# Optimization experiments

Hardware: AMD Instinct MI355X
Metric: run time of the kernel (lower is better)

## Reference

```python
import jax, jax.numpy as jnp
import numpy as np

N_CELLS_RNA, N_GENES = 8000, 8000
N_CELLS_ATAC, N_REGIONS = 8000, 20000
N_FACTORS = 100

def setup_inputs() -> dict:
    key = jax.random.key(0)
    ks = jax.random.split(key, 10)
    return {
        "G": jax.random.uniform(ks[0], (N_CELLS_RNA, N_GENES), jnp.float32),
        "R": jax.random.uniform(ks[1], (N_CELLS_ATAC, N_REGIONS), jnp.float32),
        "A": jax.random.uniform(ks[2], (N_GENES, N_REGIONS), jnp.float32),
        "C_1": jax.random.uniform(ks[3], (N_CELLS_RNA, N_FACTORS), jnp.float32),
        "C_2": jax.random.uniform(ks[4], (N_CELLS_ATAC, N_FACTORS), jnp.float32),
        "C_g": jax.random.uniform(ks[5], (N_GENES, N_FACTORS), jnp.float32),
        "C_r": jax.random.uniform(ks[6], (N_REGIONS, N_FACTORS), jnp.float32),
        "A_g": jax.random.normal(ks[7], (N_FACTORS, N_FACTORS), jnp.float32),
        "A_r": jax.random.normal(ks[8], (N_FACTORS, N_FACTORS), jnp.float32),
        "b_g": jnp.zeros((1, N_GENES), jnp.float32),
        "b_r": jnp.zeros((1, N_REGIONS), jnp.float32),
        "b_1": jnp.zeros((N_CELLS_RNA, 1), jnp.float32),
        "b_2": jnp.zeros((N_CELLS_ATAC, 1), jnp.float32),
        "alpha": jnp.array([1000.0, 1000.0, 100.0, 10.0, 0.0], jnp.float32),
    }

def reference(G, R, A, C_1, C_2, C_g, C_r, A_g, A_r, b_g, b_r, b_1, b_2, alpha):
    sm = lambda X: jax.nn.softmax(X, axis=1)  # row-wise softmax as in torch dim=1
    S1, S2, Sg, Sr = sm(C_1), sm(C_2), sm(C_g), sm(C_r)
    # loss1: RNA reconstruction. [n1,N]@[N,N] then @[N,ng]
    rec_G = (S1 @ A_g) @ Sg.T
    loss1 = jnp.mean(jnp.square(G - rec_G - b_g - b_1))
    # loss2: ATAC reconstruction
    rec_R = (S2 @ A_r) @ Sr.T
    loss2 = jnp.mean(jnp.square(R - rec_R - b_r - b_2))
    # loss3: -trace(A_r^T A_g) / ||A_r|| / ||A_g||
    loss3 = -jnp.sum(A_r * A_g) / jnp.linalg.norm(A_r) / jnp.linalg.norm(A_g)
    # loss4: -trace(Sg^T (A Sr)) / ||Sg|| / ||A Sr||  (trace via elementwise sum)
    ASr = A @ Sr  # [ng, N]
    loss4 = -jnp.sum(Sg * ASr) / jnp.linalg.norm(Sg) / jnp.linalg.norm(ASr)
    l1 = alpha[0] * loss1
    l2 = alpha[1] * loss2
    l3 = alpha[2] * loss3
    l4 = alpha[3] * loss4
    loss = l1 + l2 + l3 + l4
    return jnp.stack([loss, l1, l2, l3, l4])
```

## Files before the change

### kernel.cpp

```cpp
#include <hip/hip_runtime.h>

typedef __bf16 bf16x8 __attribute__((ext_vector_type(8)));
typedef float  f32x4  __attribute__((ext_vector_type(4)));
typedef unsigned short us4 __attribute__((ext_vector_type(4)));

#define N_CELLS 8000
#define N_GENES 8000
#define N_REG   20000
#define NF      100
#define KP      128
#define NFT     112
#define KSPLIT  5

static __device__ __forceinline__ unsigned short f2bf_bits(float f) {
  unsigned u = __builtin_bit_cast(unsigned, f);
  u = (u + 0x7FFFu + ((u >> 16) & 1u)) >> 16;
  return (unsigned short)u;
}
static __device__ __forceinline__ __bf16 f2bf(float f) {
  unsigned short h = f2bf_bits(f);
  return __builtin_bit_cast(__bf16, h);
}
static __device__ __forceinline__ float bf2f(unsigned short s) {
  unsigned u = ((unsigned)s) << 16;
  return __builtin_bit_cast(float, u);
}
static __device__ __forceinline__ bf16x8 cvt8(f32x4 v0, f32x4 v1) {
  bf16x8 r;
  r[0]=f2bf(v0[0]); r[1]=f2bf(v0[1]); r[2]=f2bf(v0[2]); r[3]=f2bf(v0[3]);
  r[4]=f2bf(v1[0]); r[5]=f2bf(v1[1]); r[6]=f2bf(v1[2]); r[7]=f2bf(v1[3]);
  return r;
}

__global__ __launch_bounds__(64) void pre_kernel(
    const float* __restrict__ C1, const float* __restrict__ C2,
    const float* __restrict__ Cg, const float* __restrict__ Cr,
    const float* __restrict__ Ag, const float* __restrict__ Ar,
    unsigned short* __restrict__ T1, unsigned short* __restrict__ T2,
    unsigned short* __restrict__ Sg, unsigned short* __restrict__ Sr,
    unsigned short* __restrict__ SrT,
    float* __restrict__ accv) {
  __shared__ float srow[NF];
  int b = blockIdx.x, t = threadIdx.x;
  if (b >= 44000) {
    float d = 0.f, na = 0.f, nr = 0.f;
    for (int i = t; i < NF * NF; i += 64) {
      float a = Ag[i], r = Ar[i];
      d = fmaf(a, r, d); na = fmaf(a, a, na); nr = fmaf(r, r, nr);
    }
    #pragma unroll
    for (int off = 32; off > 0; off >>= 1) {
      d += __shfl_xor(d, off); na += __shfl_xor(na, off); nr += __shfl_xor(nr, off);
    }
    if (t == 0) { accv[2] = d; accv[3] = na; accv[4] = nr; }
    return;
  }
  const float* C; const float* W = nullptr;
  unsigned short* outR = nullptr; unsigned short* outT = nullptr;
  bool isSr = false;
  int i;
  if (b < 8000)       { C = C1; W = Ag; outT = T1; i = b; }
  else if (b < 16000) { C = C2; W = Ar; outT = T2; i = b - 8000; }
  else if (b < 24000) { C = Cg; outR = Sg; i = b - 16000; }
  else                { C = Cr; outR = Sr; isSr = true; i = b - 24000; }

  float v0 = C[i * NF + t];
  float v1 = (t < 36) ? C[i * NF + 64 + t] : -3.0e38f;
  float m = fmaxf(v0, v1);
  #pragma unroll
  for (int off = 32; off > 0; off >>= 1) m = fmaxf(m, __shfl_xor(m, off));
  float e0 = __expf(v0 - m);
  float e1 = (t < 36) ? __expf(v1 - m) : 0.f;
  float s = e0 + e1;
  #pragma unroll
  for (int off = 32; off > 0; off >>= 1) s += __shfl_xor(s, off);
  float inv = 1.f / s;
  e0 *= inv; e1 *= inv;

  if (outT == nullptr) {
    unsigned short b0 = f2bf_bits(e0);
    unsigned short b1 = (t < 36) ? f2bf_bits(e1) : (unsigned short)0;
    outR[i * KP + t] = b0;
    outR[i * KP + 64 + t] = b1;
    if (isSr) {
      SrT[t * N_REG + i] = b0;
      if (t < 48) SrT[(64 + t) * N_REG + i] = b1;
    }
    return;
  }
  srow[t] = e0;
  if (t < 36) srow[64 + t] = e1;
  __syncthreads();
  int c2 = 64 + t;
  int c2c = (c2 < NF) ? c2 : NF - 1;
  float a0=0.f, a1=0.f, a2=0.f, a3=0.f;
  float d0=0.f, d1=0.f, d2=0.f, d3=0.f;
  #pragma unroll 4
  for (int k = 0; k < NF; k += 4) {
    float s0 = srow[k], s1 = srow[k+1], s2 = srow[k+2], s3 = srow[k+3];
    a0 = fmaf(s0, W[(k  )*NF + t], a0);
    a1 = fmaf(s1, W[(k+1)*NF + t], a1);
    a2 = fmaf(s2, W[(k+2)*NF + t], a2);
    a3 = fmaf(s3, W[(k+3)*NF + t], a3);
    d0 = fmaf(s0, W[(k  )*NF + c2c], d0);
    d1 = fmaf(s1, W[(k+1)*NF + c2c], d1);
    d2 = fmaf(s2, W[(k+2)*NF + c2c], d2);
    d3 = fmaf(s3, W[(k+3)*NF + c2c], d3);
  }
  outT[i * KP + t]  = f2bf_bits((a0 + a1) + (a2 + a3));
  outT[i * KP + c2] = (c2 < NF) ? f2bf_bits((d0 + d1) + (d2 + d3)) : (unsigned short)0;
}

__global__ __launch_bounds__(256, 3) void resid_kernel(
    const float* __restrict__ X,
    const unsigned short* __restrict__ Tm,
    const unsigned short* __restrict__ Sm,
    const float* __restrict__ bcol,
    const float* __restrict__ brow,
    int N, float* __restrict__ buckets) {
  __shared__ char ldsbuf[49152];
  char* ldsT = ldsbuf;
  char* ldsS = ldsbuf + 16384;
  int t = threadIdx.x;
  int wid = t >> 6, lane = t & 63;
  int lr = lane & 15, lg = lane >> 4;
  long r0blk = (long)blockIdx.y * 64;
  long c0blk = (long)blockIdx.x * 128;
  int r0 = (wid >> 1) * 32;
  int c0 = (wid & 1) * 64;

  bf16x8 sT[4], sS[8];
  #pragma unroll
  for (int i2 = 0; i2 < 4; ++i2) {
    int g = i2 * 256 + t, row = g >> 4, gi = g & 15;
    sT[i2] = *reinterpret_cast<const bf16x8*>(Tm + (r0blk + row) * KP + gi * 8);
  }
  #pragma unroll
  for (int i2 = 0; i2 < 8; ++i2) {
    int g = i2 * 256 + t, row = g >> 4, gi = g & 15;
    sS[i2] = *reinterpret_cast<const bf16x8*>(Sm + (c0blk + row) * KP + gi * 8);
  }

  f32x4 xv[2][4];
  #pragma unroll
  for (int ri = 0; ri < 2; ++ri) {
    long row = r0blk + r0 + ri * 16 + lr;
    #pragma unroll
    for (int ci = 0; ci < 4; ++ci) {
      long cb = c0blk + c0 + ci * 16 + lg * 4;
      if (cb < N) xv[ri][ci] = *reinterpret_cast<const f32x4*>(X + row * N + cb);
      else        xv[ri][ci] = f32x4{0.f, 0.f, 0.f, 0.f};
    }
  }

  #pragma unroll
  for (int i2 = 0; i2 < 4; ++i2) {
    int g = i2 * 256 + t, row = g >> 4, gi = g & 15;
    int off = row * 256 + ((gi * 16) ^ ((row & 7) << 4));
    *reinterpret_cast<bf16x8*>(ldsT + off) = sT[i2];
  }
  #pragma unroll
  for (int i2 = 0; i2 < 8; ++i2) {
    int g = i2 * 256 + t, row = g >> 4, gi = g & 15;
    int off = row * 256 + ((gi * 16) ^ ((row & 7) << 4));
    *reinterpret_cast<bf16x8*>(ldsS + off) = sS[i2];
  }
  __syncthreads();

  f32x4 zero = {0.f, 0.f, 0.f, 0.f};
  f32x4 acc[4][2] = {{zero, zero}, {zero, zero}, {zero, zero}, {zero, zero}};
  #pragma unroll
  for (int ks = 0; ks < 4; ++ks) {
    bf16x8 a[4], bfr[2];
    #pragma unroll
    for (int ci = 0; ci < 4; ++ci) {
      int row = c0 + ci * 16 + lr;
      int off = row * 256 + (((ks * 64) + (lg * 16)) ^ ((row & 7) << 4));
      a[ci] = *reinterpret_cast<const bf16x8*>(ldsS + off);
    }
    #pragma unroll
    for (int ri = 0; ri < 2; ++ri) {
      int row = r0 + ri * 16 + lr;
      int off = row * 256 + (((ks * 64) + (lg * 16)) ^ ((row & 7) << 4));
      bfr[ri] = *reinterpret_cast<const bf16x8*>(ldsT + off);
    }
    #pragma unroll
    for (int ci = 0; ci < 4; ++ci)
      #pragma unroll
      for (int ri = 0; ri < 2; ++ri)
        acc[ci][ri] = __builtin_amdgcn_mfma_f32_16x16x32_bf16(a[ci], bfr[ri], acc[ci][ri], 0, 0, 0);
  }

  float brv[2];
  #pragma unroll
  for (int ri = 0; ri < 2; ++ri) brv[ri] = brow[r0blk + r0 + ri * 16 + lr];

  float sse = 0.f;
  #pragma unroll
  for (int ci = 0; ci < 4; ++ci) {
    long cb = c0blk + c0 + ci * 16 + lg * 4;
    if (cb < N) {
      f32x4 bc = *reinterpret_cast<const f32x4*>(bcol + cb);
      #pragma unroll
      for (int ri = 0; ri < 2; ++ri) {
        f32x4 x = xv[ri][ci];
        #pragma unroll
        for (int j = 0; j < 4; ++j) {
          float e = x[j] - acc[ci][ri][j] - bc[j] - brv[ri];
          sse = fmaf(e, e, sse);
        }
      }
    }
  }
  #pragma unroll
  for (int off = 32; off > 0; off >>= 1) sse += __shfl_xor(sse, off);
  __shared__ float wsum[4];
  if (lane == 0) wsum[wid] = sse;
  __syncthreads();
  if (t == 0)
    atomicAdd(&buckets[(blockIdx.y * gridDim.x + blockIdx.x) & 63],
              wsum[0] + wsum[1] + wsum[2] + wsum[3]);
}

__global__ __launch_bounds__(256) void asr_kernel(
    const float* __restrict__ A,
    const unsigned short* __restrict__ SrT,
    float* __restrict__ ASr5) {
  __shared__ char lds[16384];
  int t = threadIdx.x;
  int w = t >> 6, lane = t & 63;
  int lr = lane & 15, lg = lane >> 4;
  int gBase = blockIdx.x * 64;
  int kb0 = blockIdx.y * (N_REG / KSPLIT);

  f32x4 zero = {0.f, 0.f, 0.f, 0.f};
  f32x4 acc[7] = {zero, zero, zero, zero, zero, zero, zero};

  const unsigned short* pb = SrT + (long)lr * N_REG + lg * 8;

  #pragma unroll 1
  for (int it = 0; it < 32; ++it) {
    int kb = kb0 + it * 128;
    __syncthreads();
    if (it < 31) {
      #pragma unroll
      for (int p = 0; p < 4; ++p) {
        int flat = p * 2048 + t * 8;
        int row = flat >> 7, kk = flat & 127;
        const float* src = A + (long)(gBase + row) * N_REG + kb + kk;
        f32x4 v0 = *reinterpret_cast<const f32x4*>(src);
        f32x4 v1 = *reinterpret_cast<const f32x4*>(src + 4);
        int off = row * 256 + ((kk * 2) ^ ((row & 7) << 4));
        *reinterpret_cast<bf16x8*>(lds + off) = cvt8(v0, v1);
      }
    } else {
      int row = t >> 2, kk = (t & 3) * 8;
      const float* src = A + (long)(gBase + row) * N_REG + kb + kk;
      f32x4 v0 = *reinterpret_cast<const f32x4*>(src);
      f32x4 v1 = *reinterpret_cast<const f32x4*>(src + 4);
      int off = row * 256 + ((kk * 2) ^ ((row & 7) << 4));
      *reinterpret_cast<bf16x8*>(lds + off) = cvt8(v0, v1);
    }
    __syncthreads();
    int nk = (it < 31) ? 4 : 1;
    #pragma unroll 1
    for (int ks = 0; ks < nk; ++ks) {
      int row = w * 16 + lr;
      int off = row * 256 + (((ks * 64) + lg * 16) ^ ((row & 7) << 4));
      bf16x8 ag = *reinterpret_cast<const bf16x8*>(lds + off);
      #pragma unroll
      for (int ni = 0; ni < 7; ++ni) {
        bf16x8 b = *reinterpret_cast<const bf16x8*>(pb + (long)ni * 16 * N_REG + kb + ks * 32);
        acc[ni] = __builtin_amdgcn_mfma_f32_16x16x32_bf16(ag, b, acc[ni], 0, 0, 0);
      }
    }
  }

  float* slice = ASr5 + (long)blockIdx.y * (N_GENES * NFT);
  int g0 = gBase + w * 16;
  #pragma unroll
  for (int ni = 0; ni < 7; ++ni) {
    int f = ni * 16 + lr;
    #pragma unroll
    for (int j = 0; j < 4; ++j)
      slice[(g0 + lg * 4 + j) * NFT + f] = acc[ni][j];
  }
}

__global__ void l4red_kernel(const unsigned short* __restrict__ Sgbf,
                             const float* __restrict__ ASr5,
                             float* __restrict__ accv) {
  const int NV = N_GENES * NFT / 4;
  int t = blockIdx.x * blockDim.x + threadIdx.x;
  float d = 0.f, n1 = 0.f, n2 = 0.f;
  for (int q = t; q < NV; q += gridDim.x * blockDim.x) {
    int g = q / (NFT / 4);
    int f4 = (q - g * (NFT / 4)) * 4;
    f32x4 av = {0.f, 0.f, 0.f, 0.f};
    #pragma unroll
    for (int s = 0; s < KSPLIT; ++s)
      av += *reinterpret_cast<const f32x4*>(ASr5 + (long)s * (N_GENES * NFT) + g * NFT + f4);
    us4 sgb = *reinterpret_cast<const us4*>(Sgbf + g * KP + f4);
    #pragma unroll
    for (int j = 0; j < 4; ++j) {
      float sg = bf2f(sgb[j]);
      d = fmaf(sg, av[j], d); n1 = fmaf(sg, sg, n1); n2 = fmaf(av[j], av[j], n2);
    }
  }
  #pragma unroll
  for (int off = 32; off > 0; off >>= 1) {
    d += __shfl_xor(d, off); n1 += __shfl_xor(n1, off); n2 += __shfl_xor(n2, off);
  }
  __shared__ float r3[3][4];
  int lane = threadIdx.x & 63, w = threadIdx.x >> 6;
  if (lane == 0) { r3[0][w] = d; r3[1][w] = n1; r3[2][w] = n2; }
  __syncthreads();
  if (threadIdx.x == 0) {
    atomicAdd(&accv[5], r3[0][0] + r3[0][1] + r3[0][2] + r3[0][3]);
    atomicAdd(&accv[6], r3[1][0] + r3[1][1] + r3[1][2] + r3[1][3]);
    atomicAdd(&accv[7], r3[2][0] + r3[2][1] + r3[2][2] + r3[2][3]);
  }
}

__global__ void fin_kernel(const float* __restrict__ accv,
                           const float* __restrict__ bk1,
                           const float* __restrict__ bk2,
                           const float* __restrict__ alpha,
                           float* __restrict__ out) {
  if (threadIdx.x == 0) {
    float s1 = 0.f, s2 = 0.f;
    for (int i = 0; i < 64; ++i) { s1 += bk1[i]; s2 += bk2[i]; }
    float loss1 = s1 / 64000000.0f;
    float loss2 = s2 / 160000000.0f;
    float loss3 = -accv[2] / (sqrtf(accv[3]) * sqrtf(accv[4]));
    float loss4 = -accv[5] / (sqrtf(accv[6]) * sqrtf(accv[7]));
    float l1 = alpha[0] * loss1, l2 = alpha[1] * loss2;
    float l3 = alpha[2] * loss3, l4 = alpha[3] * loss4;
    out[0] = l1 + l2 + l3 + l4;
    out[1] = l1; out[2] = l2; out[3] = l3; out[4] = l4;
  }
}


extern "C" void kernel_launch(void* const* d_in, const int* in_sizes, int n_in,
                              void* d_out, int out_size, void* d_ws, size_t ws_size,
                              hipStream_t stream) {
  const float* G  = (const float*)d_in[0];
  const float* R  = (const float*)d_in[1];
  const float* A  = (const float*)d_in[2];
  const float* C1 = (const float*)d_in[3];
  const float* C2 = (const float*)d_in[4];
  const float* Cg = (const float*)d_in[5];
  const float* Cr = (const float*)d_in[6];
  const float* Ag = (const float*)d_in[7];
  const float* Ar = (const float*)d_in[8];
  const float* bg = (const float*)d_in[9];
  const float* br = (const float*)d_in[10];
  const float* b1 = (const float*)d_in[11];
  const float* b2 = (const float*)d_in[12];
  const float* alpha = (const float*)d_in[13];

  char* ws = (char*)d_ws;
  float* accv           = (float*)(ws + 0);
  float* buckets1       = (float*)(ws + 64);
  float* buckets2       = (float*)(ws + 320);
  float* ASr5           = (float*)(ws + 1024);
  unsigned short* T1    = (unsigned short*)(ws + 17921024);
  unsigned short* T2    = (unsigned short*)(ws + 19969024);
  unsigned short* Sg    = (unsigned short*)(ws + 22017024);
  unsigned short* Sr    = (unsigned short*)(ws + 24065024);
  unsigned short* SrT   = (unsigned short*)(ws + 29185024);

  hipMemsetAsync(d_ws, 0, 576, stream);

  pre_kernel<<<44001, 64, 0, stream>>>(C1, C2, Cg, Cr, Ag, Ar,
                                       T1, T2, Sg, Sr, SrT, accv);

  resid_kernel<<<dim3(63, 125), 256, 0, stream>>>(G, T1, Sg, bg, b1, N_GENES, buckets1);
  resid_kernel<<<dim3(157, 125), 256, 0, stream>>>(R, T2, Sr, br, b2, N_REG, buckets2);

  asr_kernel<<<dim3(125, KSPLIT), 256, 0, stream>>>(A, SrT, ASr5);

  l4red_kernel<<<128, 256, 0, stream>>>(Sg, ASr5, accv);
  fin_kernel<<<1, 64, 0, stream>>>(accv, buckets1, buckets2, alpha, (float*)d_out);
}
```

Measured before the change: 671.8 us.

## Raise A@Sr split-K to 25 and double-buffer LDS with register prefetch

The A@Sr kernel now splits the 20000-long reduction into 25 chunks of 800 instead of 5 of 4000. This gives 3125 blocks instead of 625 to fill the GPU. Each block prefetches the next A tile into registers while the current tile is computed, using two LDS buffers, so one barrier per iteration is enough. The bf16 conversion now uses the library intrinsic. The cost is five times more partial-sum traffic: 25 slices of 8000x112 floats are written and then re-read by the reduction kernel, and the workspace layout grows to match.

Measured after the change: 650.5 us. 1.03x faster.

```diff
diff --git a/kernel.cpp b/kernel.cpp
--- a/kernel.cpp
+++ b/kernel.cpp
@@ -1,4 +1,5 @@
 #include <hip/hip_runtime.h>
+#include <hip/hip_bf16.h>
 
 typedef __bf16 bf16x8 __attribute__((ext_vector_type(8)));
 typedef float  f32x4  __attribute__((ext_vector_type(4)));
@@ -10,25 +11,27 @@
 #define NF      100
 #define KP      128
 #define NFT     112
-#define KSPLIT  5
+#define KSPLIT  25
 
 static __device__ __forceinline__ unsigned short f2bf_bits(float f) {
   unsigned u = __builtin_bit_cast(unsigned, f);
   u = (u + 0x7FFFu + ((u >> 16) & 1u)) >> 16;
   return (unsigned short)u;
 }
-static __device__ __forceinline__ __bf16 f2bf(float f) {
-  unsigned short h = f2bf_bits(f);
-  return __builtin_bit_cast(__bf16, h);
-}
 static __device__ __forceinline__ float bf2f(unsigned short s) {
   unsigned u = ((unsigned)s) << 16;
   return __builtin_bit_cast(float, u);
 }
-static __device__ __forceinline__ bf16x8 cvt8(f32x4 v0, f32x4 v1) {
+static __device__ __forceinline__ bf16x8 cvt8n(f32x4 v0, f32x4 v1) {
   bf16x8 r;
-  r[0]=f2bf(v0[0]); r[1]=f2bf(v0[1]); r[2]=f2bf(v0[2]); r[3]=f2bf(v0[3]);
-  r[4]=f2bf(v1[0]); r[5]=f2bf(v1[1]); r[6]=f2bf(v1[2]); r[7]=f2bf(v1[3]);
+  r[0] = __builtin_bit_cast(__bf16, __float2bfloat16(v0[0]));
+  r[1] = __builtin_bit_cast(__bf16, __float2bfloat16(v0[1]));
+  r[2] = __builtin_bit_cast(__bf16, __float2bfloat16(v0[2]));
+  r[3] = __builtin_bit_cast(__bf16, __float2bfloat16(v0[3]));
+  r[4] = __builtin_bit_cast(__bf16, __float2bfloat16(v1[0]));
+  r[5] = __builtin_bit_cast(__bf16, __float2bfloat16(v1[1]));
+  r[6] = __builtin_bit_cast(__bf16, __float2bfloat16(v1[2]));
+  r[7] = __builtin_bit_cast(__bf16, __float2bfloat16(v1[3]));
   return r;
 }
 
@@ -222,52 +225,73 @@
               wsum[0] + wsum[1] + wsum[2] + wsum[3]);
 }
 
-__global__ __launch_bounds__(256) void asr_kernel(
+__global__ __launch_bounds__(256, 4) void asr_kernel(
     const float* __restrict__ A,
     const unsigned short* __restrict__ SrT,
-    float* __restrict__ ASr5) {
-  __shared__ char lds[16384];
+    float* __restrict__ ASrN) {
+  __shared__ char lds[2][16384];
   int t = threadIdx.x;
   int w = t >> 6, lane = t & 63;
   int lr = lane & 15, lg = lane >> 4;
   int gBase = blockIdx.x * 64;
-  int kb0 = blockIdx.y * (N_REG / KSPLIT);
+  int kb0 = blockIdx.y * 800;
+
+  const unsigned short* pb = SrT + (long)lr * N_REG + lg * 8;
 
   f32x4 zero = {0.f, 0.f, 0.f, 0.f};
   f32x4 acc[7] = {zero, zero, zero, zero, zero, zero, zero};
-
-  const unsigned short* pb = SrT + (long)lr * N_REG + lg * 8;
+  f32x4 sreg[8];
+
+  #pragma unroll
+  for (int p = 0; p < 4; ++p) {
+    int flat = p * 2048 + t * 8;
+    int row = flat >> 7, kk = flat & 127;
+    const float* src = A + (long)(gBase + row) * N_REG + kb0 + kk;
+    sreg[2 * p]     = *reinterpret_cast<const f32x4*>(src);
+    sreg[2 * p + 1] = *reinterpret_cast<const f32x4*>(src + 4);
+  }
 
   #pragma unroll 1
-  for (int it = 0; it < 32; ++it) {
-    int kb = kb0 + it * 128;
-    __syncthreads();
-    if (it < 31) {
+  for (int it = 0; it < 7; ++it) {
+    char* buf = lds[it & 1];
+    if (it < 6) {
       #pragma unroll
       for (int p = 0; p < 4; ++p) {
         int flat = p * 2048 + t * 8;
         int row = flat >> 7, kk = flat & 127;
-        const float* src = A + (long)(gBase + row) * N_REG + kb + kk;
-        f32x4 v0 = *reinterpret_cast<const f32x4*>(src);
-        f32x4 v1 = *reinterpret_cast<const f32x4*>(src + 4);
         int off = row * 256 + ((kk * 2) ^ ((row & 7) << 4));
-        *reinterpret_cast<bf16x8*>(lds + off) = cvt8(v0, v1);
+        *reinterpret_cast<bf16x8*>(buf + off) = cvt8n(sreg[2 * p], sreg[2 * p + 1]);
       }
     } else {
       int row = t >> 2, kk = (t & 3) * 8;
-      const float* src = A + (long)(gBase + row) * N_REG + kb + kk;
-      f32x4 v0 = *reinterpret_cast<const f32x4*>(src);
-      f32x4 v1 = *reinterpret_cast<const f32x4*>(src + 4);
       int off = row * 256 + ((kk * 2) ^ ((row & 7) << 4));
-      *reinterpret_cast<bf16x8*>(lds + off) = cvt8(v0, v1);
+      *reinterpret_cast<bf16x8*>(buf + off) = cvt8n(sreg[0], sreg[1]);
     }
     __syncthreads();
-    int nk = (it < 31) ? 4 : 1;
-    #pragma unroll 1
+
+    if (it < 5) {
+      #pragma unroll
+      for (int p = 0; p < 4; ++p) {
+        int flat = p * 2048 + t * 8;
+        int row = flat >> 7, kk = flat & 127;
+        const float* src = A + (long)(gBase + row) * N_REG + kb0 + (it + 1) * 128 + kk;
+        sreg[2 * p]     = *reinterpret_cast<const f32x4*>(src);
+        sreg[2 * p + 1] = *reinterpret_cast<const f32x4*>(src + 4);
+      }
+    } else if (it == 5) {
+      int row = t >> 2, kk = (t & 3) * 8;
+      const float* src = A + (long)(gBase + row) * N_REG + kb0 + 768 + kk;
+      sreg[0] = *reinterpret_cast<const f32x4*>(src);
+      sreg[1] = *reinterpret_cast<const f32x4*>(src + 4);
+    }
+
+    int kb = kb0 + it * 128;
+    int arow = w * 16 + lr;
+    int nk = (it < 6) ? 4 : 1;
+    #pragma unroll 4
     for (int ks = 0; ks < nk; ++ks) {
-      int row = w * 16 + lr;
-      int off = row * 256 + (((ks * 64) + lg * 16) ^ ((row & 7) << 4));
-      bf16x8 ag = *reinterpret_cast<const bf16x8*>(lds + off);
+      int off = arow * 256 + (((ks * 64) + lg * 16) ^ ((arow & 7) << 4));
+      bf16x8 ag = *reinterpret_cast<const bf16x8*>(buf + off);
       #pragma unroll
       for (int ni = 0; ni < 7; ++ni) {
         bf16x8 b = *reinterpret_cast<const bf16x8*>(pb + (long)ni * 16 * N_REG + kb + ks * 32);
@@ -276,7 +300,7 @@
     }
   }
 
-  float* slice = ASr5 + (long)blockIdx.y * (N_GENES * NFT);
+  float* slice = ASrN + (long)blockIdx.y * (N_GENES * NFT);
   int g0 = gBase + w * 16;
   #pragma unroll
   for (int ni = 0; ni < 7; ++ni) {
@@ -288,7 +312,7 @@
 }
 
 __global__ void l4red_kernel(const unsigned short* __restrict__ Sgbf,
-                             const float* __restrict__ ASr5,
+                             const float* __restrict__ ASrN,
                              float* __restrict__ accv) {
   const int NV = N_GENES * NFT / 4;
   int t = blockIdx.x * blockDim.x + threadIdx.x;
@@ -299,7 +323,7 @@
     f32x4 av = {0.f, 0.f, 0.f, 0.f};
     #pragma unroll
     for (int s = 0; s < KSPLIT; ++s)
-      av += *reinterpret_cast<const f32x4*>(ASr5 + (long)s * (N_GENES * NFT) + g * NFT + f4);
+      av += *reinterpret_cast<const f32x4*>(ASrN + (long)s * (N_GENES * NFT) + g * NFT + f4);
     us4 sgb = *reinterpret_cast<const us4*>(Sgbf + g * KP + f4);
     #pragma unroll
     for (int j = 0; j < 4; ++j) {
@@ -364,12 +388,12 @@
   float* accv           = (float*)(ws + 0);
   float* buckets1       = (float*)(ws + 64);
   float* buckets2       = (float*)(ws + 320);
-  float* ASr5           = (float*)(ws + 1024);
-  unsigned short* T1    = (unsigned short*)(ws + 17921024);
-  unsigned short* T2    = (unsigned short*)(ws + 19969024);
-  unsigned short* Sg    = (unsigned short*)(ws + 22017024);
-  unsigned short* Sr    = (unsigned short*)(ws + 24065024);
-  unsigned short* SrT   = (unsigned short*)(ws + 29185024);
+  float* ASrN           = (float*)(ws + 1024);
+  unsigned short* T1    = (unsigned short*)(ws + 89601024);
+  unsigned short* T2    = (unsigned short*)(ws + 91649024);
+  unsigned short* Sg    = (unsigned short*)(ws + 93697024);
+  unsigned short* Sr    = (unsigned short*)(ws + 95745024);
+  unsigned short* SrT   = (unsigned short*)(ws + 100865024);
 
   hipMemsetAsync(d_ws, 0, 576, stream);
 
@@ -379,8 +403,8 @@
   resid_kernel<<<dim3(63, 125), 256, 0, stream>>>(G, T1, Sg, bg, b1, N_GENES, buckets1);
   resid_kernel<<<dim3(157, 125), 256, 0, stream>>>(R, T2, Sr, br, b2, N_REG, buckets2);
 
-  asr_kernel<<<dim3(125, KSPLIT), 256, 0, stream>>>(A, SrT, ASr5);
-
-  l4red_kernel<<<128, 256, 0, stream>>>(Sg, ASr5, accv);
+  asr_kernel<<<dim3(125, KSPLIT), 256, 0, stream>>>(A, SrT, ASrN);
+
+  l4red_kernel<<<128, 256, 0, stream>>>(Sg, ASrN, accv);
   fin_kernel<<<1, 64, 0, stream>>>(accv, buckets1, buckets2, alpha, (float*)d_out);
 }
```
